# Kernel optimization log

Hardware: AMD Instinct MI355X
Metric: run time of the kernel (lower is better)

## Reference

```python
import jax, jax.numpy as jnp
import numpy as np
import math

B, S, KV_DIM, Q_DIM, E, H = 16, 8192, 512, 512, 512, 8
D = E // H  # head_dim = 64


def setup_inputs() -> dict:
    key = jax.random.key(0)
    ks = jax.random.split(key, 12)
    s_q = 1.0 / math.sqrt(Q_DIM)
    s_kv = 1.0 / math.sqrt(KV_DIM)
    s_e = 1.0 / math.sqrt(E)
    return {
        "query": jax.random.normal(ks[0], (B, Q_DIM), dtype=jnp.float32),
        "key_value": jax.random.normal(ks[1], (B, S, KV_DIM), dtype=jnp.float32),
        "Wq": jax.random.uniform(ks[2], (Q_DIM, E), jnp.float32, -s_q, s_q),
        "bq": jax.random.uniform(ks[3], (E,), jnp.float32, -s_q, s_q),
        "Wk": jax.random.uniform(ks[4], (KV_DIM, E), jnp.float32, -s_kv, s_kv),
        "bk": jax.random.uniform(ks[5], (E,), jnp.float32, -s_kv, s_kv),
        "Wv": jax.random.uniform(ks[6], (KV_DIM, E), jnp.float32, -s_kv, s_kv),
        "bv": jax.random.uniform(ks[7], (E,), jnp.float32, -s_kv, s_kv),
        "Wo": jax.random.uniform(ks[8], (E, E), jnp.float32, -s_e, s_e),
        "bo": jax.random.uniform(ks[9], (E,), jnp.float32, -s_e, s_e),
    }


def reference(query, key_value, Wq, bq, Wk, bk, Wv, bv, Wo, bo):
    bsz, seq_len, _ = key_value.shape
    # q: [B, H, D] (single query per batch)
    q = (query @ Wq + bq).reshape(bsz, H, D)
    # k, v: [B, S, H, D]
    k = (key_value @ Wk + bk).reshape(bsz, seq_len, H, D)
    v = (key_value @ Wv + bv).reshape(bsz, seq_len, H, D)
    scale = 1.0 / math.sqrt(D)
    # attn logits: [B, H, S]
    attn = jnp.einsum("bhd,bshd->bhs", q, k) * scale
    weights = jax.nn.softmax(attn, axis=-1)
    # context: [B, H, D] -> [B, E]
    context = jnp.einsum("bhs,bshd->bhd", weights, v).reshape(bsz, E)
    return context @ Wo + bo
```

## Files before the change

### kernel.cpp

```cpp
#include <hip/hip_runtime.h>
#include <math.h>

#define B_   16
#define S_   8192
#define KVD  512
#define E_   512
#define H_   8
#define D_   64

#define OFF_QKVEC   0
#define OFF_LACC    65536
#define OFF_CTXACC  65664
#define OFF_CTXBUF  131200
#define ZERO_START  OFF_LACC
#define ZERO_COUNT  73856

__global__ __launch_bounds__(256) void k_prep(const float* __restrict__ query,
                                              const float* __restrict__ Wq,
                                              const float* __restrict__ bq,
                                              const float* __restrict__ Wk,
                                              float* __restrict__ wsf,
                                              float* __restrict__ out) {
    const int blk = blockIdx.x;
    const int tid = threadIdx.x;

    if (blk >= 64) {
        int i = (blk - 64) * 256 + tid;
        const int nws4 = ZERO_COUNT / 4;
        if (i < nws4) {
            *(float4*)&wsf[ZERO_START + i * 4] = make_float4(0.f, 0.f, 0.f, 0.f);
        } else if (i < nws4 + (B_ * E_) / 4) {
            *(float4*)&out[(size_t)(i - nws4) * 4] = make_float4(0.f, 0.f, 0.f, 0.f);
        }
        return;
    }

    const int cc = blk & 7, h = blk >> 3;
    float* qk_vec = wsf + OFF_QKVEC;

    __shared__ float qbuf[16 * 512];
    __shared__ float wk[64 * 65];
    __shared__ float qh[16 * 64];

    #pragma unroll
    for (int k = 0; k < 8; ++k) {
        int f4i = tid + k * 256;
        *(float4*)&qbuf[f4i * 4] = *(const float4*)&query[(size_t)f4i * 4];
    }
    #pragma unroll
    for (int k = 0; k < 4; ++k) {
        int f4i = tid + k * 256;
        int row = f4i >> 4, d4 = f4i & 15;
        float4 v = *(const float4*)&Wk[(size_t)(cc * 64 + row) * E_ + h * D_ + d4 * 4];
        wk[row * 65 + d4 * 4 + 0] = v.x;
        wk[row * 65 + d4 * 4 + 1] = v.y;
        wk[row * 65 + d4 * 4 + 2] = v.z;
        wk[row * 65 + d4 * 4 + 3] = v.w;
    }
    __syncthreads();

    const int d = tid & 63, w = tid >> 6;
    {
        float acc[4] = {0.f, 0.f, 0.f, 0.f};
        const float* wq = Wq + h * D_ + d;
        for (int k = 0; k < 512; k += 4) {
            #pragma unroll
            for (int kk = 0; kk < 4; ++kk) {
                float wv = wq[(size_t)(k + kk) * E_];
                #pragma unroll
                for (int i = 0; i < 4; ++i)
                    acc[i] = fmaf(qbuf[(w * 4 + i) * 512 + k + kk], wv, acc[i]);
            }
        }
        float bqv = bq[h * D_ + d];
        #pragma unroll
        for (int i = 0; i < 4; ++i)
            qh[(w * 4 + i) * 64 + d] = (acc[i] + bqv) * 0.125f;
    }
    __syncthreads();

    {
        const int c_local = tid & 63;
        float acc[4] = {0.f, 0.f, 0.f, 0.f};
        for (int dd = 0; dd < 64; ++dd) {
            float wv = wk[c_local * 65 + dd];
            #pragma unroll
            for (int i = 0; i < 4; ++i)
                acc[i] = fmaf(qh[(w * 4 + i) * 64 + dd], wv, acc[i]);
        }
        #pragma unroll
        for (int i = 0; i < 4; ++i) {
            int b = w * 4 + i;
            qk_vec[((size_t)b * H_ + h) * KVD + cc * 64 + c_local] = acc[i];
        }
    }
}

#define SROW 68
#define RB   2

__device__ __forceinline__ void attn_loadrows(float (&kvr)[RB][8],
                                              const float* __restrict__ base,
                                              int it, int lane) {
    #pragma unroll
    for (int r = 0; r < RB; ++r) {
        const float* rowp = base + (size_t)(it * RB + r) * KVD;
        float4 v0 = *(const float4*)&rowp[lane * 4];
        float4 v1 = *(const float4*)&rowp[256 + lane * 4];
        kvr[r][0] = v0.x; kvr[r][1] = v0.y; kvr[r][2] = v0.z; kvr[r][3] = v0.w;
        kvr[r][4] = v1.x; kvr[r][5] = v1.y; kvr[r][6] = v1.z; kvr[r][7] = v1.w;
    }
}

__device__ __forceinline__ void attn_process(const float (&kvr)[RB][8],
                                             const float (&qk)[H_][8],
                                             float (&ctx)[H_][8], float& l_run,
                                             float* wscr, int lane) {
    const int seg = lane & 7;
    const int hme = lane >> 3;
    #pragma unroll
    for (int r = 0; r < RB; ++r)
        #pragma unroll
        for (int h = 0; h < H_; ++h) {
            float p = 0.f;
            #pragma unroll
            for (int j = 0; j < 8; ++j) p = fmaf(kvr[r][j], qk[h][j], p);
            wscr[(r * H_ + h) * SROW + lane] = p;
        }
    asm volatile("" ::: "memory");
    const float* rdb = wscr + hme * SROW + seg * 8;
    float e4[RB];
    #pragma unroll
    for (int r = 0; r < RB; ++r) {
        const float* p = rdb + r * H_ * SROW;
        float4 x = *(const float4*)p;
        float4 y = *(const float4*)(p + 4);
        float s = ((x.x + x.y) + (x.z + x.w)) + ((y.x + y.y) + (y.z + y.w));
        s += __shfl_xor(s, 1);
        s += __shfl_xor(s, 2);
        s += __shfl_xor(s, 4);
        e4[r] = __expf(s);
        l_run += e4[r];
    }
    #pragma unroll
    for (int r = 0; r < RB; ++r)
        #pragma unroll
        for (int h = 0; h < H_; ++h) {
            float wv = __shfl(e4[r], h * 8 + seg);
            #pragma unroll
            for (int j = 0; j < 8; ++j)
                ctx[h][j] = fmaf(wv, kvr[r][j], ctx[h][j]);
        }
}

template <int NC>
__global__ __launch_bounds__(256, 2) void k_attn(const float* __restrict__ kv,
                                                 const float* __restrict__ qk_vec,
                                                 float* __restrict__ ctx_acc,
                                                 float* __restrict__ l_acc) {
    constexpr int CHUNK = S_ / NC;
    constexpr int RPW = CHUNK / 4;
    constexpr int NIT = RPW / RB;
    constexpr int SPW = RB * H_ * SROW;

    __shared__ __align__(16) float scr[4 * SPW];
    __shared__ float lbuf[32];

    const int tid = threadIdx.x;
    const int lane = tid & 63;
    const int w = tid >> 6;
    const int nc = blockIdx.x, b = blockIdx.y;
    const int hme = lane >> 3, seg = lane & 7;

    float qk[H_][8];
    {
        const float* qb = qk_vec + (size_t)b * H_ * KVD;
        #pragma unroll
        for (int h = 0; h < H_; ++h) {
            float4 v0 = *(const float4*)&qb[h * KVD + lane * 4];
            float4 v1 = *(const float4*)&qb[h * KVD + 256 + lane * 4];
            qk[h][0] = v0.x; qk[h][1] = v0.y; qk[h][2] = v0.z; qk[h][3] = v0.w;
            qk[h][4] = v1.x; qk[h][5] = v1.y; qk[h][6] = v1.z; qk[h][7] = v1.w;
        }
    }

    float ctx[H_][8];
    #pragma unroll
    for (int h = 0; h < H_; ++h)
        #pragma unroll
        for (int j = 0; j < 8; ++j) ctx[h][j] = 0.f;
    float l_run = 0.f;

    float* wscr = scr + w * SPW;
    const float* kvbase = kv + ((size_t)b * S_ + (size_t)nc * CHUNK + (size_t)w * RPW) * KVD;

    float kvA[RB][8], kvB[RB][8];
    attn_loadrows(kvA, kvbase, 0, lane);
    #pragma unroll 1
    for (int it = 0; it < NIT; it += 2) {
        attn_loadrows(kvB, kvbase, it + 1, lane);
        attn_process(kvA, qk, ctx, l_run, wscr, lane);
        if (it + 2 < NIT) attn_loadrows(kvA, kvbase, it + 2, lane);
        attn_process(kvB, qk, ctx, l_run, wscr, lane);
    }

    if (seg == 0) lbuf[w * 8 + hme] = l_run;
    __syncthreads();
    float* cbuf = scr;
    if (w == 0) {
        #pragma unroll
        for (int h = 0; h < H_; ++h) {
            *(float4*)&cbuf[h * KVD + lane * 4] =
                make_float4(ctx[h][0], ctx[h][1], ctx[h][2], ctx[h][3]);
            *(float4*)&cbuf[h * KVD + 256 + lane * 4] =
                make_float4(ctx[h][4], ctx[h][5], ctx[h][6], ctx[h][7]);
        }
    }
    __syncthreads();
    if (w != 0) {
        #pragma unroll
        for (int h = 0; h < H_; ++h) {
            #pragma unroll
            for (int j = 0; j < 4; ++j)
                atomicAdd(&cbuf[h * KVD + lane * 4 + j], ctx[h][j]);
            #pragma unroll
            for (int j = 4; j < 8; ++j)
                atomicAdd(&cbuf[h * KVD + 256 + lane * 4 + (j - 4)], ctx[h][j]);
        }
    }
    __syncthreads();
    size_t gbase = (size_t)b * (H_ * KVD);
    #pragma unroll
    for (int k = 0; k < 16; ++k)
        atomicAdd(&ctx_acc[gbase + k * 256 + tid], cbuf[k * 256 + tid]);
    if (tid < H_) {
        float L = lbuf[tid] + lbuf[8 + tid] + lbuf[16 + tid] + lbuf[24 + tid];
        atomicAdd(&l_acc[b * H_ + tid], L);
    }
}

__global__ __launch_bounds__(512) void k_ctx(const float* __restrict__ ctx_acc,
                                             const float* __restrict__ l_acc,
                                             const float* __restrict__ Wv,
                                             const float* __restrict__ bv,
                                             float* __restrict__ ctx_buf) {
    const int kc = blockIdx.x, b = blockIdx.y;
    const int e = threadIdx.x;
    const int h = e >> 6;
    const float inv = 1.0f / l_acc[b * H_ + h];
    const float* ca = ctx_acc + ((size_t)b * H_ + h) * KVD + kc * 128;
    const float* wv = Wv + (size_t)(kc * 128) * E_ + e;
    float a0 = 0.f, a1 = 0.f, a2 = 0.f, a3 = 0.f;
    for (int c = 0; c < 128; c += 4) {
        a0 = fmaf(ca[c],     wv[(size_t)(c)     * E_], a0);
        a1 = fmaf(ca[c + 1], wv[(size_t)(c + 1) * E_], a1);
        a2 = fmaf(ca[c + 2], wv[(size_t)(c + 2) * E_], a2);
        a3 = fmaf(ca[c + 3], wv[(size_t)(c + 3) * E_], a3);
    }
    float val = ((a0 + a1) + (a2 + a3)) * inv;
    if (kc == 0) val += bv[e];
    atomicAdd(&ctx_buf[(size_t)b * E_ + e], val);
}

__global__ __launch_bounds__(512) void k_o(const float* __restrict__ ctx_buf,
                                           const float* __restrict__ Wo,
                                           const float* __restrict__ bo,
                                           float* __restrict__ out) {
    const int kc = blockIdx.x, b = blockIdx.y;
    const int e = threadIdx.x;
    const float* cs = ctx_buf + (size_t)b * E_ + kc * 128;
    const float* wo = Wo + (size_t)(kc * 128) * E_ + e;
    float a0 = 0.f, a1 = 0.f, a2 = 0.f, a3 = 0.f;
    for (int k = 0; k < 128; k += 4) {
        a0 = fmaf(cs[k],     wo[(size_t)(k)     * E_], a0);
        a1 = fmaf(cs[k + 1], wo[(size_t)(k + 1) * E_], a1);
        a2 = fmaf(cs[k + 2], wo[(size_t)(k + 2) * E_], a2);
        a3 = fmaf(cs[k + 3], wo[(size_t)(k + 3) * E_], a3);
    }
    float val = (a0 + a1) + (a2 + a3);
    if (kc == 0) val += bo[e];
    atomicAdd(&out[(size_t)b * E_ + e], val);
}

extern "C" void kernel_launch(void* const* d_in, const int* in_sizes, int n_in,
                              void* d_out, int out_size, void* d_ws, size_t ws_size,
                              hipStream_t stream) {
    const float* query = (const float*)d_in[0];
    const float* kv    = (const float*)d_in[1];
    const float* Wq    = (const float*)d_in[2];
    const float* bq    = (const float*)d_in[3];
    const float* Wk    = (const float*)d_in[4];
    const float* Wv    = (const float*)d_in[6];
    const float* bv    = (const float*)d_in[7];
    const float* Wo    = (const float*)d_in[8];
    const float* bo    = (const float*)d_in[9];
    float* out = (float*)d_out;
    float* wsf = (float*)d_ws;

    float* qk_vec  = wsf + OFF_QKVEC;
    float* l_acc   = wsf + OFF_LACC;
    float* ctx_acc = wsf + OFF_CTXACC;
    float* ctx_buf = wsf + OFF_CTXBUF;

    constexpr int NC = 32;

    k_prep<<<145, 256, 0, stream>>>(query, Wq, bq, Wk, wsf, out);
    k_attn<NC><<<dim3(NC, B_), 256, 0, stream>>>(kv, qk_vec, ctx_acc, l_acc);
    k_ctx<<<dim3(4, B_), 512, 0, stream>>>(ctx_acc, l_acc, Wv, bv, ctx_buf);
    k_o<<<dim3(4, B_), 512, 0, stream>>>(ctx_buf, Wo, bo, out);
}
```

Baseline: 449.0 us.

## Stage key/value rows through a three-deep LDS ring with async global-to-LDS loads

Replaces the register double-buffered key/value row loads with a per-wave three-stage shared-memory ring, filled by direct global-to-LDS async loads (`global_load_lds`). A manual `s_waitcnt vmcnt(8)` gates each slot before it is read. The aim is to keep more loads in flight and hide memory latency without tying up registers. In exchange it adds about 48KB of LDS per block. The fixed wait count does not shrink in the tail iterations, so the last slots may be read before their loads land. The ds reads from a slot are also not fenced before that slot is re-filled.

```diff
diff --git a/kernel.cpp b/kernel.cpp
--- a/kernel.cpp
+++ b/kernel.cpp
@@ -98,17 +98,21 @@
 
 #define SROW 68
 #define RB   2
-
-__device__ __forceinline__ void attn_loadrows(float (&kvr)[RB][8],
-                                              const float* __restrict__ base,
-                                              int it, int lane) {
+#define NSTAGE 3
+
+__device__ __forceinline__ void stage_slot(const float* base, int it,
+                                           float* slot, int lane) {
     #pragma unroll
     for (int r = 0; r < RB; ++r) {
         const float* rowp = base + (size_t)(it * RB + r) * KVD;
-        float4 v0 = *(const float4*)&rowp[lane * 4];
-        float4 v1 = *(const float4*)&rowp[256 + lane * 4];
-        kvr[r][0] = v0.x; kvr[r][1] = v0.y; kvr[r][2] = v0.z; kvr[r][3] = v0.w;
-        kvr[r][4] = v1.x; kvr[r][5] = v1.y; kvr[r][6] = v1.z; kvr[r][7] = v1.w;
+        __builtin_amdgcn_global_load_lds(
+            (__attribute__((address_space(1))) unsigned int*)(rowp + lane * 4),
+            (__attribute__((address_space(3))) unsigned int*)(slot + r * 512),
+            16, 0, 0);
+        __builtin_amdgcn_global_load_lds(
+            (__attribute__((address_space(1))) unsigned int*)(rowp + 256 + lane * 4),
+            (__attribute__((address_space(3))) unsigned int*)(slot + r * 512 + 256),
+            16, 0, 0);
     }
 }
 
@@ -162,7 +166,9 @@
     constexpr int RPW = CHUNK / 4;
     constexpr int NIT = RPW / RB;
     constexpr int SPW = RB * H_ * SROW;
-
+    constexpr int SLOT = RB * 512;
+
+    __shared__ __align__(16) float ring[4][NSTAGE][SLOT];
     __shared__ __align__(16) float scr[4 * SPW];
     __shared__ float lbuf[32];
 
@@ -192,16 +198,29 @@
     float l_run = 0.f;
 
     float* wscr = scr + w * SPW;
+    float* myring = &ring[w][0][0];
     const float* kvbase = kv + ((size_t)b * S_ + (size_t)nc * CHUNK + (size_t)w * RPW) * KVD;
 
-    float kvA[RB][8], kvB[RB][8];
-    attn_loadrows(kvA, kvbase, 0, lane);
+    stage_slot(kvbase, 0, myring + 0 * SLOT, lane);
+    stage_slot(kvbase, 1, myring + 1 * SLOT, lane);
+    stage_slot(kvbase, 2, myring + 2 * SLOT, lane);
+
+    int sl = 0;
     #pragma unroll 1
-    for (int it = 0; it < NIT; it += 2) {
-        attn_loadrows(kvB, kvbase, it + 1, lane);
-        attn_process(kvA, qk, ctx, l_run, wscr, lane);
-        if (it + 2 < NIT) attn_loadrows(kvA, kvbase, it + 2, lane);
-        attn_process(kvB, qk, ctx, l_run, wscr, lane);
+    for (int it = 0; it < NIT; ++it) {
+        asm volatile("s_waitcnt vmcnt(8)" ::: "memory");
+        float* slot = myring + sl * SLOT;
+        float kvr[RB][8];
+        #pragma unroll
+        for (int r = 0; r < RB; ++r) {
+            float4 v0 = *(const float4*)&slot[r * 512 + lane * 4];
+            float4 v1 = *(const float4*)&slot[r * 512 + 256 + lane * 4];
+            kvr[r][0] = v0.x; kvr[r][1] = v0.y; kvr[r][2] = v0.z; kvr[r][3] = v0.w;
+            kvr[r][4] = v1.x; kvr[r][5] = v1.y; kvr[r][6] = v1.z; kvr[r][7] = v1.w;
+        }
+        if (it + NSTAGE < NIT) stage_slot(kvbase, it + NSTAGE, slot, lane);
+        attn_process(kvr, qk, ctx, l_run, wscr, lane);
+        sl = (sl + 1 == NSTAGE) ? 0 : sl + 1;
     }
 
     if (seg == 0) lbuf[w * 8 + hme] = l_run;
```

New measurement: 449.7 us. Within noise of the previous version (+0.2%).

## Stage KV tiles into LDS via async global_load_lds and split heads across waves

Applied to the files above, without the earlier changes.

The attention kernel now double-buffers 8-row KV tiles in shared memory using direct global-to-LDS loads, overlapping the next tile's fetch with compute on the current one. Each wave handles two heads over all rows instead of all heads over a quarter of the rows. This cuts register pressure and removes the cross-wave ctx reduction in shared memory. The cost is a block-wide barrier per tile and 32KB of LDS per block, which may limit occupancy. Every wave also rereads each tile from LDS.

```diff
diff --git a/kernel.cpp b/kernel.cpp
--- a/kernel.cpp
+++ b/kernel.cpp
@@ -97,60 +97,24 @@
 }
 
 #define SROW 68
-#define RB   2
-
-__device__ __forceinline__ void attn_loadrows(float (&kvr)[RB][8],
-                                              const float* __restrict__ base,
-                                              int it, int lane) {
+#define T_   8
+
+__device__ __forceinline__ void stage_tile(const float* __restrict__ chunkbase,
+                                           int t, float (&buf)[T_][KVD],
+                                           int w, int lane) {
     #pragma unroll
-    for (int r = 0; r < RB; ++r) {
-        const float* rowp = base + (size_t)(it * RB + r) * KVD;
-        float4 v0 = *(const float4*)&rowp[lane * 4];
-        float4 v1 = *(const float4*)&rowp[256 + lane * 4];
-        kvr[r][0] = v0.x; kvr[r][1] = v0.y; kvr[r][2] = v0.z; kvr[r][3] = v0.w;
-        kvr[r][4] = v1.x; kvr[r][5] = v1.y; kvr[r][6] = v1.z; kvr[r][7] = v1.w;
-    }
-}
-
-__device__ __forceinline__ void attn_process(const float (&kvr)[RB][8],
-                                             const float (&qk)[H_][8],
-                                             float (&ctx)[H_][8], float& l_run,
-                                             float* wscr, int lane) {
-    const int seg = lane & 7;
-    const int hme = lane >> 3;
-    #pragma unroll
-    for (int r = 0; r < RB; ++r)
-        #pragma unroll
-        for (int h = 0; h < H_; ++h) {
-            float p = 0.f;
-            #pragma unroll
-            for (int j = 0; j < 8; ++j) p = fmaf(kvr[r][j], qk[h][j], p);
-            wscr[(r * H_ + h) * SROW + lane] = p;
-        }
-    asm volatile("" ::: "memory");
-    const float* rdb = wscr + hme * SROW + seg * 8;
-    float e4[RB];
-    #pragma unroll
-    for (int r = 0; r < RB; ++r) {
-        const float* p = rdb + r * H_ * SROW;
-        float4 x = *(const float4*)p;
-        float4 y = *(const float4*)(p + 4);
-        float s = ((x.x + x.y) + (x.z + x.w)) + ((y.x + y.y) + (y.z + y.w));
-        s += __shfl_xor(s, 1);
-        s += __shfl_xor(s, 2);
-        s += __shfl_xor(s, 4);
-        e4[r] = __expf(s);
-        l_run += e4[r];
-    }
-    #pragma unroll
-    for (int r = 0; r < RB; ++r)
-        #pragma unroll
-        for (int h = 0; h < H_; ++h) {
-            float wv = __shfl(e4[r], h * 8 + seg);
-            #pragma unroll
-            for (int j = 0; j < 8; ++j)
-                ctx[h][j] = fmaf(wv, kvr[r][j], ctx[h][j]);
-        }
+    for (int r = 0; r < 2; ++r) {
+        const int row = w * 2 + r;
+        const float* rowp = chunkbase + (size_t)(t * T_ + row) * KVD;
+        __builtin_amdgcn_global_load_lds(
+            (__attribute__((address_space(1))) unsigned int*)(rowp + lane * 4),
+            (__attribute__((address_space(3))) unsigned int*)(&buf[row][0]),
+            16, 0, 0);
+        __builtin_amdgcn_global_load_lds(
+            (__attribute__((address_space(1))) unsigned int*)(rowp + 256 + lane * 4),
+            (__attribute__((address_space(3))) unsigned int*)(&buf[row][256]),
+            16, 0, 0);
+    }
 }
 
 template <int NC>
@@ -159,83 +123,117 @@
                                                  float* __restrict__ ctx_acc,
                                                  float* __restrict__ l_acc) {
     constexpr int CHUNK = S_ / NC;
-    constexpr int RPW = CHUNK / 4;
-    constexpr int NIT = RPW / RB;
-    constexpr int SPW = RB * H_ * SROW;
-
-    __shared__ __align__(16) float scr[4 * SPW];
-    __shared__ float lbuf[32];
+    constexpr int NT = CHUNK / T_;
+
+    __shared__ __align__(16) float kbuf[2][T_][KVD];
+    __shared__ __align__(16) float scr[4][8][SROW];
 
     const int tid = threadIdx.x;
     const int lane = tid & 63;
     const int w = tid >> 6;
     const int nc = blockIdx.x, b = blockIdx.y;
     const int hme = lane >> 3, seg = lane & 7;
-
-    float qk[H_][8];
-    {
-        const float* qb = qk_vec + (size_t)b * H_ * KVD;
-        #pragma unroll
-        for (int h = 0; h < H_; ++h) {
-            float4 v0 = *(const float4*)&qb[h * KVD + lane * 4];
-            float4 v1 = *(const float4*)&qb[h * KVD + 256 + lane * 4];
-            qk[h][0] = v0.x; qk[h][1] = v0.y; qk[h][2] = v0.z; qk[h][3] = v0.w;
-            qk[h][4] = v1.x; qk[h][5] = v1.y; qk[h][6] = v1.z; qk[h][7] = v1.w;
-        }
-    }
-
-    float ctx[H_][8];
+    const int g_mine = hme >> 1;
+    (void)g_mine;
+
+    float qk2[2][8];
+    {
+        const float* qb = qk_vec + ((size_t)b * H_ + 2 * w) * KVD;
+        #pragma unroll
+        for (int hh = 0; hh < 2; ++hh) {
+            float4 v0 = *(const float4*)&qb[hh * KVD + lane * 4];
+            float4 v1 = *(const float4*)&qb[hh * KVD + 256 + lane * 4];
+            qk2[hh][0] = v0.x; qk2[hh][1] = v0.y; qk2[hh][2] = v0.z; qk2[hh][3] = v0.w;
+            qk2[hh][4] = v1.x; qk2[hh][5] = v1.y; qk2[hh][6] = v1.z; qk2[hh][7] = v1.w;
+        }
+    }
+
+    float ctx2[2][8];
     #pragma unroll
-    for (int h = 0; h < H_; ++h)
-        #pragma unroll
-        for (int j = 0; j < 8; ++j) ctx[h][j] = 0.f;
-    float l_run = 0.f;
-
-    float* wscr = scr + w * SPW;
-    const float* kvbase = kv + ((size_t)b * S_ + (size_t)nc * CHUNK + (size_t)w * RPW) * KVD;
-
-    float kvA[RB][8], kvB[RB][8];
-    attn_loadrows(kvA, kvbase, 0, lane);
+    for (int hh = 0; hh < 2; ++hh)
+        #pragma unroll
+        for (int j = 0; j < 8; ++j) ctx2[hh][j] = 0.f;
+    float l_loc = 0.f;
+
+    const float* chunkbase = kv + ((size_t)b * S_ + (size_t)nc * CHUNK) * KVD;
+
+    stage_tile(chunkbase, 0, kbuf[0], w, lane);
+    __syncthreads();
+
+    int p = 0;
     #pragma unroll 1
-    for (int it = 0; it < NIT; it += 2) {
-        attn_loadrows(kvB, kvbase, it + 1, lane);
-        attn_process(kvA, qk, ctx, l_run, wscr, lane);
-        if (it + 2 < NIT) attn_loadrows(kvA, kvbase, it + 2, lane);
-        attn_process(kvB, qk, ctx, l_run, wscr, lane);
-    }
-
-    if (seg == 0) lbuf[w * 8 + hme] = l_run;
-    __syncthreads();
-    float* cbuf = scr;
-    if (w == 0) {
-        #pragma unroll
-        for (int h = 0; h < H_; ++h) {
-            *(float4*)&cbuf[h * KVD + lane * 4] =
-                make_float4(ctx[h][0], ctx[h][1], ctx[h][2], ctx[h][3]);
-            *(float4*)&cbuf[h * KVD + 256 + lane * 4] =
-                make_float4(ctx[h][4], ctx[h][5], ctx[h][6], ctx[h][7]);
-        }
-    }
-    __syncthreads();
-    if (w != 0) {
-        #pragma unroll
-        for (int h = 0; h < H_; ++h) {
+    for (int t = 0; t < NT; ++t) {
+        if (t + 1 < NT) stage_tile(chunkbase, t + 1, kbuf[p ^ 1], w, lane);
+        #pragma unroll
+        for (int g2 = 0; g2 < 2; ++g2) {
+            const float(&rows)[T_][KVD] = kbuf[p];
+            float kvr[4][8];
+            #pragma unroll
+            for (int r = 0; r < 4; ++r) {
+                const float* rp = &rows[g2 * 4 + r][0];
+                float4 v0 = *(const float4*)&rp[lane * 4];
+                float4 v1 = *(const float4*)&rp[256 + lane * 4];
+                kvr[r][0] = v0.x; kvr[r][1] = v0.y; kvr[r][2] = v0.z; kvr[r][3] = v0.w;
+                kvr[r][4] = v1.x; kvr[r][5] = v1.y; kvr[r][6] = v1.z; kvr[r][7] = v1.w;
+            }
+            #pragma unroll
+            for (int r = 0; r < 4; ++r)
+                #pragma unroll
+                for (int hh = 0; hh < 2; ++hh) {
+                    float pp = 0.f;
+                    #pragma unroll
+                    for (int j = 0; j < 8; ++j)
+                        pp = fmaf(kvr[r][j], qk2[hh][j], pp);
+                    scr[w][r * 2 + hh][lane] = pp;
+                }
+            asm volatile("" ::: "memory");
+            const float* gp = &scr[w][hme][seg * 8];
+            float4 x = *(const float4*)gp;
+            float4 y = *(const float4*)(gp + 4);
+            float s = ((x.x + x.y) + (x.z + x.w)) + ((y.x + y.y) + (y.z + y.w));
+            s += __shfl_xor(s, 1);
+            s += __shfl_xor(s, 2);
+            s += __shfl_xor(s, 4);
+            float e = __expf(s);
+            l_loc += e;
+            #pragma unroll
+            for (int r = 0; r < 4; ++r)
+                #pragma unroll
+                for (int hh = 0; hh < 2; ++hh) {
+                    float wv = __shfl(e, (r * 2 + hh) * 8 + seg);
+                    #pragma unroll
+                    for (int j = 0; j < 8; ++j)
+                        ctx2[hh][j] = fmaf(wv, kvr[r][j], ctx2[hh][j]);
+                }
+        }
+        __syncthreads();
+        p ^= 1;
+    }
+
+    {
+        float ls = l_loc;
+        ls += __shfl_xor(ls, 1);
+        ls += __shfl_xor(ls, 2);
+        ls += __shfl_xor(ls, 4);
+        ls += __shfl_xor(ls, 16);
+        ls += __shfl_xor(ls, 32);
+        ls *= 0.125f;
+        if (lane == 0) atomicAdd(&l_acc[b * H_ + 2 * w], ls);
+        if (lane == 8) atomicAdd(&l_acc[b * H_ + 2 * w + 1], ls);
+    }
+
+    {
+        size_t gb = (size_t)b * (H_ * KVD);
+        #pragma unroll
+        for (int hh = 0; hh < 2; ++hh) {
+            float* dst = &ctx_acc[gb + (size_t)(2 * w + hh) * KVD];
             #pragma unroll
             for (int j = 0; j < 4; ++j)
-                atomicAdd(&cbuf[h * KVD + lane * 4 + j], ctx[h][j]);
+                atomicAdd(&dst[lane * 4 + j], ctx2[hh][j]);
             #pragma unroll
             for (int j = 4; j < 8; ++j)
-                atomicAdd(&cbuf[h * KVD + 256 + lane * 4 + (j - 4)], ctx[h][j]);
-        }
-    }
-    __syncthreads();
-    size_t gbase = (size_t)b * (H_ * KVD);
-    #pragma unroll
-    for (int k = 0; k < 16; ++k)
-        atomicAdd(&ctx_acc[gbase + k * 256 + tid], cbuf[k * 256 + tid]);
-    if (tid < H_) {
-        float L = lbuf[tid] + lbuf[8 + tid] + lbuf[16 + tid] + lbuf[24 + tid];
-        atomicAdd(&l_acc[b * H_ + tid], L);
+                atomicAdd(&dst[256 + lane * 4 + (j - 4)], ctx2[hh][j]);
+        }
     }
 }
 
```

Result: faster. 432.4 us (-3.7%).
